# Kernel optimization log

Hardware: AMD Instinct MI355X
Metric: run time of the kernel (lower is better)

Reference implementation:

```python
import jax, jax.numpy as jnp
import numpy as np

B = 128        # batch (images/texts)
N = 2048       # other texts per image
F_IMG = 1024   # raw image feature dim (abstracted encoder input)
F_TXT = 512    # raw text feature dim
D = 512        # embedding dim (num_features=512 in BasicNet)
TOPK = B - 1   # default topK = batch - 1


def setup_inputs() -> dict:
    key = jax.random.key(0)
    ks = jax.random.split(key, 6)
    return {
        "input_images": jax.random.normal(ks[0], (B, F_IMG), jnp.float32),
        "input_texts": jax.random.normal(ks[1], (B, F_TXT), jnp.float32),
        "other_texts": jax.random.normal(ks[2], (B, N, F_TXT), jnp.float32),
        "W_img": jax.random.normal(ks[3], (F_IMG, D), jnp.float32) / np.float32(np.sqrt(F_IMG)),
        "W_txt": jax.random.normal(ks[4], (F_TXT, D), jnp.float32) / np.float32(np.sqrt(F_TXT)),
        "logit_scale": jnp.asarray(np.log(1.0 / 0.07), jnp.float32),
    }


def reference(input_images, input_texts, other_texts, W_img, W_txt, logit_scale):
    K = TOPK
    # encoders abstracted as linear projections to D=512
    img = input_images @ W_img                                   # [B, D]
    img = img / jnp.linalg.norm(img, axis=1, keepdims=True)      # L2-normalize images
    txt = input_texts @ W_txt                                    # [B, D]
    txt = txt / jnp.linalg.norm(txt, axis=1, keepdims=True)      # row-wise norm == norm after concat
    oth = jnp.einsum('bnf,fd->bnd', other_texts, W_txt)          # [B, N, D]
    oth = oth / jnp.linalg.norm(oth, axis=2, keepdims=True)

    scale = jnp.exp(logit_scale)
    logit_in = scale * jnp.sum(img * txt, axis=1)                # [B] image_i . text_i
    logit_oth = scale * jnp.einsum('bd,bnd->bn', img, oth)       # [B, N]

    # descending sort + take top-K (lax.top_k returns sorted descending)
    topk_vals, _ = jax.lax.top_k(logit_oth, K)                   # [B, K]

    # indices = sorted(range(K) + [min(i, K-1)]): duplicate element p=min(i,K-1)
    rows = jnp.arange(B)
    cols = jnp.arange(K + 1)[None, :]                            # [1, K+1]
    p = jnp.minimum(rows, K - 1)[:, None]                        # [B, 1]
    gidx = jnp.where(cols <= p, cols, cols - 1)                  # [B, K+1]
    gathered = jnp.take_along_axis(topk_vals, gidx, axis=1)      # [B, K+1]

    # overwrite column i of row i with the positive (input text) logit
    out = jnp.where(cols == rows[:, None], logit_in[:, None], gathered)
    return out
```

## Files before the change

kernel.cpp:

```cpp
#include <hip/hip_runtime.h>
#include <hip/hip_bf16.h>
#include <math.h>

#define B_SZ 128
#define N_OTH 2048
#define F_IMG 1024
#define F_TXT 512
#define D_EMB 512

typedef __attribute__((ext_vector_type(8))) short short8;
typedef __attribute__((ext_vector_type(16))) float f32x16;

static __device__ __forceinline__ ushort f2bf(float f) {
    __hip_bfloat16 h = __float2bfloat16(f);
    return *reinterpret_cast<ushort*>(&h);
}

__global__ __launch_bounds__(512) void k_enc(const float* __restrict__ in_img,
                                             const float* __restrict__ in_txt,
                                             const float* __restrict__ W_img,
                                             const float* __restrict__ W_txt,
                                             const float* __restrict__ p_ls,
                                             float* __restrict__ img,
                                             float* __restrict__ logit_in) {
    const int b = blockIdx.x;
    const int d = threadIdx.x;
    __shared__ float row[F_IMG];
    __shared__ float wsum[8];
    __shared__ float s_rn;
    const int lane = d & 63, wv = d >> 6;

    for (int i = d; i < F_IMG; i += 512) row[i] = in_img[b * F_IMG + i];
    __syncthreads();
    float acc = 0.f;
#pragma unroll 8
    for (int f = 0; f < F_IMG; ++f) acc = fmaf(row[f], W_img[f * D_EMB + d], acc);
    float sq = acc * acc;
#pragma unroll
    for (int off = 32; off > 0; off >>= 1) sq += __shfl_down(sq, off);
    if (lane == 0) wsum[wv] = sq;
    __syncthreads();
    if (d == 0) {
        float s = 0.f;
        for (int w = 0; w < 8; ++w) s += wsum[w];
        s_rn = 1.0f / sqrtf(s);
    }
    __syncthreads();
    const float iv = acc * s_rn;
    img[b * D_EMB + d] = iv;

    __syncthreads();
    row[d] = in_txt[b * F_TXT + d];
    __syncthreads();
    float tacc = 0.f;
#pragma unroll 8
    for (int f = 0; f < F_TXT; ++f) tacc = fmaf(row[f], W_txt[f * D_EMB + d], tacc);
    float tsq = tacc * tacc;
#pragma unroll
    for (int off = 32; off > 0; off >>= 1) tsq += __shfl_down(tsq, off);
    __syncthreads();
    if (lane == 0) wsum[wv] = tsq;
    __syncthreads();
    if (d == 0) {
        float s = 0.f;
        for (int w = 0; w < 8; ++w) s += wsum[w];
        s_rn = 1.0f / sqrtf(s);
    }
    __syncthreads();
    float pd = (tacc * s_rn) * iv;
#pragma unroll
    for (int off = 32; off > 0; off >>= 1) pd += __shfl_down(pd, off);
    __syncthreads();
    if (lane == 0) wsum[wv] = pd;
    __syncthreads();
    if (d == 0) {
        float s = 0.f;
        for (int w = 0; w < 8; ++w) s += wsum[w];
        logit_in[b] = expf(p_ls[0]) * s;
    }
}

__global__ __launch_bounds__(256) void k_wprep(const float* __restrict__ W,
                                               ushort* __restrict__ wf) {
    const int g = blockIdx.x * 256 + threadIdx.x;
    const int l = g & 63;
    const int frag = g >> 6;
    const int kstep = frag >> 4;
    const int ct = frag & 15;
    const int col = ct * 32 + (l & 31);
    const int kb = kstep * 16 + (l >> 5) * 8;
    short8 o;
#pragma unroll
    for (int j = 0; j < 8; ++j) o[j] = (short)f2bf(W[(kb + j) * D_EMB + col]);
    *(short8*)(wf + (size_t)g * 8) = o;
}

__global__ __launch_bounds__(256, 2) void k_gemm(const float* __restrict__ oth,
                                                 const ushort* __restrict__ wf,
                                                 const float* __restrict__ img,
                                                 float* __restrict__ numA,
                                                 float* __restrict__ denA) {
    __shared__ ushort sA[2][64 * 64];
    __shared__ float redN[4][64];
    __shared__ float redD[4][64];
    const int tid = threadIdx.x;
    const int l = tid & 63;
    const int wv = tid >> 6;
    const int b = blockIdx.x >> 5;
    const size_t row0 = (size_t)blockIdx.x * 64;

    const int srow = tid >> 2;
    const int sk0 = (tid & 3) * 16;
    const float* gsrc = oth + (row0 + srow) * F_TXT + sk0;
    const int swz = (srow & 7) << 4;
    const int wb0 = srow * 128 + ((sk0 * 2 + 0) ^ swz);
    const int wb1 = srow * 128 + ((sk0 * 2 + 16) ^ swz);

    const ushort* wbase = wf + ((size_t)(wv * 4) * 64 + l) * 8;

    int rowbase[2];
#pragma unroll
    for (int m = 0; m < 2; ++m) rowbase[m] = (m * 32 + (l & 31)) * 128;
    int koff[4];
#pragma unroll
    for (int ks = 0; ks < 4; ++ks) koff[ks] = ((ks * 32 + (l >> 5) * 16) ^ ((l & 7) << 4));

    f32x16 acc[2][4];
#pragma unroll
    for (int m = 0; m < 2; ++m)
#pragma unroll
        for (int n = 0; n < 4; ++n)
#pragma unroll
            for (int r = 0; r < 16; ++r) acc[m][n][r] = 0.f;

    {
        float4 v0 = *(const float4*)(gsrc + 0);
        float4 v1 = *(const float4*)(gsrc + 4);
        float4 v2 = *(const float4*)(gsrc + 8);
        float4 v3 = *(const float4*)(gsrc + 12);
        short8 p0, p1;
        p0[0] = (short)f2bf(v0.x); p0[1] = (short)f2bf(v0.y); p0[2] = (short)f2bf(v0.z); p0[3] = (short)f2bf(v0.w);
        p0[4] = (short)f2bf(v1.x); p0[5] = (short)f2bf(v1.y); p0[6] = (short)f2bf(v1.z); p0[7] = (short)f2bf(v1.w);
        p1[0] = (short)f2bf(v2.x); p1[1] = (short)f2bf(v2.y); p1[2] = (short)f2bf(v2.z); p1[3] = (short)f2bf(v2.w);
        p1[4] = (short)f2bf(v3.x); p1[5] = (short)f2bf(v3.y); p1[6] = (short)f2bf(v3.z); p1[7] = (short)f2bf(v3.w);
        *(short8*)((char*)sA[0] + wb0) = p0;
        *(short8*)((char*)sA[0] + wb1) = p1;
    }
    __syncthreads();

    for (int t = 0; t < 8; ++t) {
        const int cur = t & 1;
        short8 bfr[4][4];
#pragma unroll
        for (int ks = 0; ks < 4; ++ks)
#pragma unroll
            for (int n = 0; n < 4; ++n)
                bfr[ks][n] = *(const short8*)(wbase + (size_t)((t * 4 + ks) * 8192 + n * 512));
        __builtin_amdgcn_sched_barrier(0);
        float4 nv0, nv1, nv2, nv3;
        if (t < 7) {
            const float* gs = gsrc + (t + 1) * 64;
            nv0 = *(const float4*)(gs + 0);
            nv1 = *(const float4*)(gs + 4);
            nv2 = *(const float4*)(gs + 8);
            nv3 = *(const float4*)(gs + 12);
        }
        __builtin_amdgcn_sched_barrier(0);
#pragma unroll
        for (int ks = 0; ks < 4; ++ks) {
            short8 af[2];
#pragma unroll
            for (int m = 0; m < 2; ++m)
                af[m] = *(const short8*)((const char*)sA[cur] + rowbase[m] + koff[ks]);
#pragma unroll
            for (int m = 0; m < 2; ++m)
#pragma unroll
                for (int n = 0; n < 4; ++n)
                    acc[m][n] = __builtin_amdgcn_mfma_f32_32x32x16_bf16(af[m], bfr[ks][n], acc[m][n], 0, 0, 0);
        }
        if (t < 7) {
            short8 p0, p1;
            p0[0] = (short)f2bf(nv0.x); p0[1] = (short)f2bf(nv0.y); p0[2] = (short)f2bf(nv0.z); p0[3] = (short)f2bf(nv0.w);
            p0[4] = (short)f2bf(nv1.x); p0[5] = (short)f2bf(nv1.y); p0[6] = (short)f2bf(nv1.z); p0[7] = (short)f2bf(nv1.w);
            p1[0] = (short)f2bf(nv2.x); p1[1] = (short)f2bf(nv2.y); p1[2] = (short)f2bf(nv2.z); p1[3] = (short)f2bf(nv2.w);
            p1[4] = (short)f2bf(nv3.x); p1[5] = (short)f2bf(nv3.y); p1[6] = (short)f2bf(nv3.z); p1[7] = (short)f2bf(nv3.w);
            *(short8*)((char*)sA[cur ^ 1] + wb0) = p0;
            *(short8*)((char*)sA[cur ^ 1] + wb1) = p1;
        }
        __syncthreads();
    }

    float ic[4];
#pragma unroll
    for (int n = 0; n < 4; ++n)
        ic[n] = img[b * D_EMB + wv * 128 + n * 32 + (l & 31)];
#pragma unroll
    for (int m = 0; m < 2; ++m) {
#pragma unroll
        for (int rg = 0; rg < 16; ++rg) {
            float tn = 0.f, td = 0.f;
#pragma unroll
            for (int n = 0; n < 4; ++n) {
                const float p = acc[m][n][rg];
                tn = fmaf(p, ic[n], tn);
                td = fmaf(p, p, td);
            }
#pragma unroll
            for (int off = 1; off <= 16; off <<= 1) {
                tn += __shfl_xor(tn, off);
                td += __shfl_xor(td, off);
            }
            if ((l & 31) == 0) {
                const int r = m * 32 + (rg & 3) + 8 * (rg >> 2) + 4 * (l >> 5);
                redN[wv][r] = tn;
                redD[wv][r] = td;
            }
        }
    }
    __syncthreads();
    if (tid < 64) {
        float tn = 0.f, td = 0.f;
#pragma unroll
        for (int w = 0; w < 4; ++w) { tn += redN[w][tid]; td += redD[w][tid]; }
        numA[row0 + tid] = tn;
        denA[row0 + tid] = td;
    }
}

__global__ __launch_bounds__(512) void k_topk(const float* __restrict__ numA,
                                              const float* __restrict__ denA,
                                              const float* __restrict__ logit_in,
                                              const float* __restrict__ p_ls,
                                              float* __restrict__ out) {
    const int b = blockIdx.x;
    const int tid = threadIdx.x;
    const float scale = expf(p_ls[0]);
    __shared__ float a[N_OTH];
    for (int i = tid; i < N_OTH; i += 512) {
        const float nu = numA[(size_t)b * N_OTH + i];
        const float de = denA[(size_t)b * N_OTH + i];
        a[i] = scale * nu / sqrtf(de);
    }
    __syncthreads();
    for (unsigned k = 2; k <= N_OTH; k <<= 1) {
        for (unsigned j = k >> 1; j > 0; j >>= 1) {
#pragma unroll
            for (int s = 0; s < N_OTH / 512; ++s) {
                const unsigned i = tid + s * 512u;
                const unsigned ixj = i ^ j;
                if (ixj > i) {
                    const bool asc = ((i & k) == 0);
                    const float x = a[i], y = a[ixj];
                    if ((x > y) == asc) { a[i] = y; a[ixj] = x; }
                }
            }
            __syncthreads();
        }
    }
    if (tid < 128) {
        const int j = tid;
        float v;
        if (j == b) {
            v = logit_in[b];
        } else {
            const int m = j - (j > b ? 1 : 0);
            v = a[N_OTH - 1 - m];
        }
        out[b * 128 + j] = v;
    }
}

extern "C" void kernel_launch(void* const* d_in, const int* in_sizes, int n_in,
                              void* d_out, int out_size, void* d_ws, size_t ws_size,
                              hipStream_t stream) {
    const float* in_img = (const float*)d_in[0];
    const float* in_txt = (const float*)d_in[1];
    const float* oth    = (const float*)d_in[2];
    const float* W_img  = (const float*)d_in[3];
    const float* W_txt  = (const float*)d_in[4];
    const float* p_ls   = (const float*)d_in[5];
    float* out = (float*)d_out;

    float* ws = (float*)d_ws;
    float* img      = ws;
    float* logit_in = ws + 65536;
    float* numA     = ws + 65536 + 128;
    float* denA     = numA + 262144;
    ushort* wfrag   = (ushort*)(denA + 262144);

    k_wprep<<<128, 256, 0, stream>>>(W_txt, wfrag);
    k_enc<<<B_SZ, 512, 0, stream>>>(in_img, in_txt, W_img, W_txt, p_ls, img, logit_in);
    k_gemm<<<(B_SZ * N_OTH) / 64, 256, 0, stream>>>(oth, wfrag, img, numA, denA);
    k_topk<<<B_SZ, 512, 0, stream>>>(numA, denA, logit_in, p_ls, out);
}
```

Baseline: 335.0 us.

## Triple-buffer GEMM A tiles with two-ahead prefetch and merge prep kernels

The GEMM's A-tile staging moves from double to triple buffering in LDS. Global loads are issued two K-steps ahead into alternating register sets, and the per-step __syncthreads is replaced by an explicit lgkmcnt wait plus s_barrier, with raised wave priority around the MFMA block. The weight-fragment prep kernel is folded into the encoder kernel as extra blocks, saving one launch. The aim is to hide HBM latency of the large fp32 input stream, at the cost of more registers and LDS that could pressure 2-block occupancy.

After: 337.8 us. No clear change (+0.8%).

```diff
diff --git a/kernel.cpp b/kernel.cpp
--- a/kernel.cpp
+++ b/kernel.cpp
@@ -16,13 +16,28 @@
     return *reinterpret_cast<ushort*>(&h);
 }
 
-__global__ __launch_bounds__(512) void k_enc(const float* __restrict__ in_img,
-                                             const float* __restrict__ in_txt,
-                                             const float* __restrict__ W_img,
-                                             const float* __restrict__ W_txt,
-                                             const float* __restrict__ p_ls,
-                                             float* __restrict__ img,
-                                             float* __restrict__ logit_in) {
+__global__ __launch_bounds__(512) void k_prep(const float* __restrict__ in_img,
+                                              const float* __restrict__ in_txt,
+                                              const float* __restrict__ W_img,
+                                              const float* __restrict__ W_txt,
+                                              const float* __restrict__ p_ls,
+                                              float* __restrict__ img,
+                                              float* __restrict__ logit_in,
+                                              ushort* __restrict__ wf) {
+    if (blockIdx.x >= B_SZ) {
+        const int g = (blockIdx.x - B_SZ) * 512 + threadIdx.x;
+        const int l = g & 63;
+        const int frag = g >> 6;
+        const int kstep = frag >> 4;
+        const int ct = frag & 15;
+        const int col = ct * 32 + (l & 31);
+        const int kb = kstep * 16 + (l >> 5) * 8;
+        short8 o;
+#pragma unroll
+        for (int j = 0; j < 8; ++j) o[j] = (short)f2bf(W_txt[(kb + j) * D_EMB + col]);
+        *(short8*)(wf + (size_t)g * 8) = o;
+        return;
+    }
     const int b = blockIdx.x;
     const int d = threadIdx.x;
     __shared__ float row[F_IMG];
@@ -80,19 +95,20 @@
     }
 }
 
-__global__ __launch_bounds__(256) void k_wprep(const float* __restrict__ W,
-                                               ushort* __restrict__ wf) {
-    const int g = blockIdx.x * 256 + threadIdx.x;
-    const int l = g & 63;
-    const int frag = g >> 6;
-    const int kstep = frag >> 4;
-    const int ct = frag & 15;
-    const int col = ct * 32 + (l & 31);
-    const int kb = kstep * 16 + (l >> 5) * 8;
-    short8 o;
-#pragma unroll
-    for (int j = 0; j < 8; ++j) o[j] = (short)f2bf(W[(kb + j) * D_EMB + col]);
-    *(short8*)(wf + (size_t)g * 8) = o;
+__device__ __forceinline__ void loadA(const float* gs, float4 v[4]) {
+    v[0] = *(const float4*)(gs + 0);
+    v[1] = *(const float4*)(gs + 4);
+    v[2] = *(const float4*)(gs + 8);
+    v[3] = *(const float4*)(gs + 12);
+}
+__device__ __forceinline__ void cvtWrite(char* buf, int wb0, int wb1, const float4 v[4]) {
+    short8 p0, p1;
+    p0[0] = (short)f2bf(v[0].x); p0[1] = (short)f2bf(v[0].y); p0[2] = (short)f2bf(v[0].z); p0[3] = (short)f2bf(v[0].w);
+    p0[4] = (short)f2bf(v[1].x); p0[5] = (short)f2bf(v[1].y); p0[6] = (short)f2bf(v[1].z); p0[7] = (short)f2bf(v[1].w);
+    p1[0] = (short)f2bf(v[2].x); p1[1] = (short)f2bf(v[2].y); p1[2] = (short)f2bf(v[2].z); p1[3] = (short)f2bf(v[2].w);
+    p1[4] = (short)f2bf(v[3].x); p1[5] = (short)f2bf(v[3].y); p1[6] = (short)f2bf(v[3].z); p1[7] = (short)f2bf(v[3].w);
+    *(short8*)(buf + wb0) = p0;
+    *(short8*)(buf + wb1) = p1;
 }
 
 __global__ __launch_bounds__(256, 2) void k_gemm(const float* __restrict__ oth,
@@ -100,7 +116,7 @@
                                                  const float* __restrict__ img,
                                                  float* __restrict__ numA,
                                                  float* __restrict__ denA) {
-    __shared__ ushort sA[2][64 * 64];
+    __shared__ ushort sA[3][64 * 64];
     __shared__ float redN[4][64];
     __shared__ float redD[4][64];
     const int tid = threadIdx.x;
@@ -133,61 +149,54 @@
 #pragma unroll
             for (int r = 0; r < 16; ++r) acc[m][n][r] = 0.f;
 
-    {
-        float4 v0 = *(const float4*)(gsrc + 0);
-        float4 v1 = *(const float4*)(gsrc + 4);
-        float4 v2 = *(const float4*)(gsrc + 8);
-        float4 v3 = *(const float4*)(gsrc + 12);
-        short8 p0, p1;
-        p0[0] = (short)f2bf(v0.x); p0[1] = (short)f2bf(v0.y); p0[2] = (short)f2bf(v0.z); p0[3] = (short)f2bf(v0.w);
-        p0[4] = (short)f2bf(v1.x); p0[5] = (short)f2bf(v1.y); p0[6] = (short)f2bf(v1.z); p0[7] = (short)f2bf(v1.w);
-        p1[0] = (short)f2bf(v2.x); p1[1] = (short)f2bf(v2.y); p1[2] = (short)f2bf(v2.z); p1[3] = (short)f2bf(v2.w);
-        p1[4] = (short)f2bf(v3.x); p1[5] = (short)f2bf(v3.y); p1[6] = (short)f2bf(v3.z); p1[7] = (short)f2bf(v3.w);
-        *(short8*)((char*)sA[0] + wb0) = p0;
-        *(short8*)((char*)sA[0] + wb1) = p1;
-    }
-    __syncthreads();
-
+    float4 va[4], vb[4];
+    loadA(gsrc + 0 * 64, va);
+    loadA(gsrc + 1 * 64, vb);
+    __builtin_amdgcn_sched_barrier(0);
+    cvtWrite((char*)sA[0], wb0, wb1, va);
+    asm volatile("s_waitcnt lgkmcnt(0)" ::: "memory");
+    __builtin_amdgcn_sched_barrier(0);
+    __builtin_amdgcn_s_barrier();
+    __builtin_amdgcn_sched_barrier(0);
+
+#pragma unroll
     for (int t = 0; t < 8; ++t) {
-        const int cur = t & 1;
         short8 bfr[4][4];
 #pragma unroll
-        for (int ks = 0; ks < 4; ++ks)
+        for (int ks = 0; ks < 4; ++ks) {
+            const ushort* bptr = wbase + (size_t)(t * 4 + ks) * 8192;
 #pragma unroll
             for (int n = 0; n < 4; ++n)
-                bfr[ks][n] = *(const short8*)(wbase + (size_t)((t * 4 + ks) * 8192 + n * 512));
+                bfr[ks][n] = *(const short8*)(bptr + n * 512);
+        }
         __builtin_amdgcn_sched_barrier(0);
-        float4 nv0, nv1, nv2, nv3;
-        if (t < 7) {
-            const float* gs = gsrc + (t + 1) * 64;
-            nv0 = *(const float4*)(gs + 0);
-            nv1 = *(const float4*)(gs + 4);
-            nv2 = *(const float4*)(gs + 8);
-            nv3 = *(const float4*)(gs + 12);
+        if (t < 6) {
+            if ((t & 1) == 0) loadA(gsrc + (t + 2) * 64, va);
+            else              loadA(gsrc + (t + 2) * 64, vb);
         }
         __builtin_amdgcn_sched_barrier(0);
+        __builtin_amdgcn_s_setprio(1);
 #pragma unroll
         for (int ks = 0; ks < 4; ++ks) {
             short8 af[2];
 #pragma unroll
             for (int m = 0; m < 2; ++m)
-                af[m] = *(const short8*)((const char*)sA[cur] + rowbase[m] + koff[ks]);
+                af[m] = *(const short8*)((const char*)sA[t % 3] + rowbase[m] + koff[ks]);
 #pragma unroll
             for (int m = 0; m < 2; ++m)
 #pragma unroll
                 for (int n = 0; n < 4; ++n)
                     acc[m][n] = __builtin_amdgcn_mfma_f32_32x32x16_bf16(af[m], bfr[ks][n], acc[m][n], 0, 0, 0);
         }
+        __builtin_amdgcn_s_setprio(0);
         if (t < 7) {
-            short8 p0, p1;
-            p0[0] = (short)f2bf(nv0.x); p0[1] = (short)f2bf(nv0.y); p0[2] = (short)f2bf(nv0.z); p0[3] = (short)f2bf(nv0.w);
-            p0[4] = (short)f2bf(nv1.x); p0[5] = (short)f2bf(nv1.y); p0[6] = (short)f2bf(nv1.z); p0[7] = (short)f2bf(nv1.w);
-            p1[0] = (short)f2bf(nv2.x); p1[1] = (short)f2bf(nv2.y); p1[2] = (short)f2bf(nv2.z); p1[3] = (short)f2bf(nv2.w);
-            p1[4] = (short)f2bf(nv3.x); p1[5] = (short)f2bf(nv3.y); p1[6] = (short)f2bf(nv3.z); p1[7] = (short)f2bf(nv3.w);
-            *(short8*)((char*)sA[cur ^ 1] + wb0) = p0;
-            *(short8*)((char*)sA[cur ^ 1] + wb1) = p1;
-        }
-        __syncthreads();
+            if ((t & 1) == 0) cvtWrite((char*)sA[(t + 1) % 3], wb0, wb1, vb);
+            else              cvtWrite((char*)sA[(t + 1) % 3], wb0, wb1, va);
+        }
+        asm volatile("s_waitcnt lgkmcnt(0)" ::: "memory");
+        __builtin_amdgcn_sched_barrier(0);
+        __builtin_amdgcn_s_barrier();
+        __builtin_amdgcn_sched_barrier(0);
     }
 
     float ic[4];
@@ -288,8 +297,7 @@
     float* denA     = numA + 262144;
     ushort* wfrag   = (ushort*)(denA + 262144);
 
-    k_wprep<<<128, 256, 0, stream>>>(W_txt, wfrag);
-    k_enc<<<B_SZ, 512, 0, stream>>>(in_img, in_txt, W_img, W_txt, p_ls, img, logit_in);
+    k_prep<<<B_SZ + 64, 512, 0, stream>>>(in_img, in_txt, W_img, W_txt, p_ls, img, logit_in, wfrag);
     k_gemm<<<(B_SZ * N_OTH) / 64, 256, 0, stream>>>(oth, wfrag, img, numA, denA);
     k_topk<<<B_SZ, 512, 0, stream>>>(numA, denA, logit_in, p_ls, out);
 }
```
